# Performance work log

Measured on AMD Instinct MI355X. Metric: run time of the kernel, lower is better.

The kernel has to match this reference:

```python
import jax, jax.numpy as jnp
import numpy as np

D_MODEL = 1024
N_HEADS = 16
HEAD_DIM = D_MODEL // N_HEADS


def setup_inputs() -> dict:
    key = jax.random.key(0)
    ks = jax.random.split(key, 9)
    s = 1.0 / np.sqrt(D_MODEL)
    return {
        "x": jax.random.normal(ks[0], (4, 2048, D_MODEL), dtype=jnp.float32),
        "Wq": jax.random.normal(ks[1], (D_MODEL, D_MODEL), dtype=jnp.float32) * s,
        "bq": jax.random.normal(ks[2], (D_MODEL,), dtype=jnp.float32) * 0.01,
        "Wk": jax.random.normal(ks[3], (D_MODEL, D_MODEL), dtype=jnp.float32) * s,
        "bk": jax.random.normal(ks[4], (D_MODEL,), dtype=jnp.float32) * 0.01,
        "Wv": jax.random.normal(ks[5], (D_MODEL, D_MODEL), dtype=jnp.float32) * s,
        "bv": jax.random.normal(ks[6], (D_MODEL,), dtype=jnp.float32) * 0.01,
        "Wo": jax.random.normal(ks[7], (D_MODEL, D_MODEL), dtype=jnp.float32) * s,
        "bo": jax.random.normal(ks[8], (D_MODEL,), dtype=jnp.float32) * 0.01,
    }


def reference(x, Wq, bq, Wk, bk, Wv, bv, Wo, bo):
    b, s, d = x.shape  # [batch, seq, d_model]
    # projections (weights stored as [d_in, d_out], equiv to torch Linear W.T)
    q = x @ Wq + bq
    k = x @ Wk + bk
    v = x @ Wv + bv
    # split heads -> [b, h, s, hd]
    q = q.reshape(b, s, N_HEADS, HEAD_DIM).transpose(0, 2, 1, 3)
    k = k.reshape(b, s, N_HEADS, HEAD_DIM).transpose(0, 2, 1, 3)
    v = v.reshape(b, s, N_HEADS, HEAD_DIM).transpose(0, 2, 1, 3)
    scale = 1.0 / jnp.sqrt(jnp.asarray(HEAD_DIM, dtype=q.dtype))
    scores = jnp.einsum("bhqd,bhkd->bhqk", q, k) * scale  # [b,h,s,s]
    attn = jax.nn.softmax(scores, axis=-1)
    y = jnp.einsum("bhqk,bhkd->bhqd", attn, v)
    y = y.transpose(0, 2, 1, 3).reshape(b, s, d)
    return y @ Wo + bo
```

## Files before the change

### kernel.cpp

```cpp
#include <hip/hip_runtime.h>

#define SEQ   2048
#define DM    1024
#define NH    16
#define HD    64
#define MTOT  8192
#define QSCALE 0.18033688011112042f
#define SMAX  12.0f

typedef _Float16 f16x8 __attribute__((ext_vector_type(8)));
typedef float    f32x4 __attribute__((ext_vector_type(4)));

__device__ __forceinline__ unsigned short f2h(float f) {
    _Float16 h = (_Float16)f;
    return __builtin_bit_cast(unsigned short, h);
}
__device__ __forceinline__ float h2f(unsigned short u) {
    return (float)__builtin_bit_cast(_Float16, u);
}
__device__ __forceinline__ unsigned int pkrtz(float a, float b) {
    return __builtin_bit_cast(unsigned int, __builtin_amdgcn_cvt_pkrtz(a, b));
}
__device__ __forceinline__ float fexp2(float x) {
    return __builtin_amdgcn_exp2f(x);
}
__device__ __forceinline__ void async_cp16(const void* g, void* l) {
    __builtin_amdgcn_global_load_lds(
        (const __attribute__((address_space(1))) unsigned int*)g,
        (__attribute__((address_space(3))) unsigned int*)l, 16, 0, 0);
}

__global__ __launch_bounds__(256) void convert_x_kernel(
    const float* __restrict__ x, unsigned short* __restrict__ Xh)
{
    const size_t i8 = ((size_t)blockIdx.x * 256 + threadIdx.x) * 8;
    float f[8];
    *(float4*)&f[0] = *(const float4*)(x + i8);
    *(float4*)&f[4] = *(const float4*)(x + i8 + 4);
    unsigned short h[8];
#pragma unroll
    for (int e = 0; e < 8; ++e) h[e] = f2h(f[e]);
    uint4 ph;
    ph.x = h[0] | ((unsigned)h[1] << 16); ph.y = h[2] | ((unsigned)h[3] << 16);
    ph.z = h[4] | ((unsigned)h[5] << 16); ph.w = h[6] | ((unsigned)h[7] << 16);
    *(uint4*)(Xh + i8) = ph;
}

__global__ __launch_bounds__(256) void convert_w_kernel(
    const float* __restrict__ Wq, const float* __restrict__ Wk,
    const float* __restrict__ Wv, const float* __restrict__ Wo,
    unsigned short* __restrict__ WTh, unsigned short* __restrict__ WTl)
{
    __shared__ float tile[32][33];
    const int z = blockIdx.z;
    const float* W = (z == 0) ? Wq : (z == 1) ? Wk : (z == 2) ? Wv : Wo;
    const float s = (z == 0) ? QSCALE : 1.0f;
    const int r0 = blockIdx.y << 5, c0 = blockIdx.x << 5;
    const int tx = threadIdx.x, ty = threadIdx.y;
#pragma unroll
    for (int u = 0; u < 4; ++u)
        tile[ty + 8 * u][tx] = W[(size_t)(r0 + ty + 8 * u) * DM + c0 + tx];
    __syncthreads();
#pragma unroll
    for (int u = 0; u < 4; ++u) {
        const int dout = c0 + ty + 8 * u;
        const int din  = r0 + tx;
        const float v = tile[tx][ty + 8 * u] * s;
        const unsigned short hh = f2h(v);
        const size_t idx = (size_t)(z * DM + dout) * DM + din;
        WTh[idx] = hh;
        if (z == 3) WTl[idx] = f2h(v - h2f(hh));
    }
}

__global__ __launch_bounds__(256, 3) void gemm_kernel(
    const unsigned short* __restrict__ Agh, const unsigned short* __restrict__ Agl,
    const unsigned short* __restrict__ Bgh, const unsigned short* __restrict__ Bgl,
    const float* __restrict__ b0, const float* __restrict__ b1,
    const float* __restrict__ b2,
    float* __restrict__ Cf,
    unsigned short* __restrict__ Qf, unsigned short* __restrict__ Kf,
    unsigned short* __restrict__ Vt,
    const int mode)
{
    __shared__ unsigned short gsm[16384];

    const int t = threadIdx.x;
    const int wave = t >> 6, L = t & 63;
    const int quad = L >> 4, l16 = L & 15;
    const int m0 = blockIdx.x << 7, n0 = blockIdx.y << 7;

    const int trl = L >> 2;
    const int ck  = (L & 3) ^ (trl & 3);
    const unsigned short* gsrc;
    unsigned short* lb;
    int ub;
    if (mode == 1) {
        gsrc = (wave < 2) ? Agh : Bgh;
        ub   = (wave & 1) << 2;
        lb   = &gsm[((wave >> 1) << 13) + ((wave & 1) << 11)];
    } else {
        gsrc = (wave == 0) ? Agh : (wave == 1) ? Agl
             : (wave == 2) ? Bgh : Bgl;
        ub   = 0;
        lb   = &gsm[wave << 12];
    }
    const int rbase = (wave < 2) ? m0 : n0;
    const unsigned short* gl = gsrc + (size_t)(rbase + trl) * DM + ck * 8;

    const int wm = (wave >> 1) << 6, wn = (wave & 1) << 6;
    const int xk2 = l16 & 3;
    f32x4 acc[4][4] = {};

    for (int k0 = 0; k0 < DM; k0 += 32) {
        __syncthreads();
        if (mode == 1) {
#pragma unroll
            for (int u = 0; u < 4; ++u)
                async_cp16(gl + (size_t)(ub + u) * 16 * DM + k0, lb + (u << 9));
        } else {
#pragma unroll
            for (int u = 0; u < 8; ++u)
                async_cp16(gl + (size_t)u * 16 * DM + k0, lb + (u << 9));
        }
        __syncthreads();

        f16x8 fah[4], fal[4], fbh[4], fbl[4];
#pragma unroll
        for (int i = 0; i < 4; ++i) {
            const int ao = (wm + (i << 4) + l16) * 32 + ((quad ^ xk2) << 3);
            fah[i] = *(const f16x8*)&gsm[ao];
        }
#pragma unroll
        for (int j = 0; j < 4; ++j) {
            const int bo_ = (wn + (j << 4) + l16) * 32 + ((quad ^ xk2) << 3);
            fbh[j] = *(const f16x8*)&gsm[8192 + bo_];
        }
        if (mode == 0) {
#pragma unroll
            for (int i = 0; i < 4; ++i) {
                const int ao = (wm + (i << 4) + l16) * 32 + ((quad ^ xk2) << 3);
                fal[i] = *(const f16x8*)&gsm[4096 + ao];
            }
#pragma unroll
            for (int j = 0; j < 4; ++j) {
                const int bo_ = (wn + (j << 4) + l16) * 32 + ((quad ^ xk2) << 3);
                fbl[j] = *(const f16x8*)&gsm[12288 + bo_];
            }
        }
#pragma unroll
        for (int i = 0; i < 4; ++i)
#pragma unroll
            for (int j = 0; j < 4; ++j) {
                acc[i][j] = __builtin_amdgcn_mfma_f32_16x16x32_f16(fah[i], fbh[j], acc[i][j], 0, 0, 0);
                if (mode == 0) {
                    acc[i][j] = __builtin_amdgcn_mfma_f32_16x16x32_f16(fal[i], fbh[j], acc[i][j], 0, 0, 0);
                    acc[i][j] = __builtin_amdgcn_mfma_f32_16x16x32_f16(fah[i], fbl[j], acc[i][j], 0, 0, 0);
                }
            }
    }

    if (mode == 0) {
#pragma unroll
        for (int j = 0; j < 4; ++j) {
            const int col = n0 + wn + (j << 4) + l16;
            const float bj = b0[col];
#pragma unroll
            for (int i = 0; i < 4; ++i)
#pragma unroll
                for (int r = 0; r < 4; ++r) {
                    const int row = m0 + wm + (i << 4) + (quad << 2) + r;
                    Cf[(size_t)row * DM + col] = acc[i][j][r] + bj;
                }
        }
    } else {
#pragma unroll
        for (int j = 0; j < 4; ++j) {
            const int col = n0 + wn + (j << 4) + l16;
            const int seg = col >> 10;
            const int c = col & 1023;
            const int h_ = c >> 6, d_ = c & 63;
            const float bj = (seg == 0) ? b0[c] * QSCALE : (seg == 1) ? b1[c] : b2[c];
            unsigned short* Op = (seg == 0) ? Qf : Kf;
#pragma unroll
            for (int i = 0; i < 4; ++i) {
                const int row0 = m0 + wm + (i << 4) + (quad << 2);
                const int b_ = row0 >> 11, s0 = row0 & 2047;
                if (seg < 2) {
                    const size_t ib = ((size_t)b_ * NH + h_) * SEQ;
#pragma unroll
                    for (int r = 0; r < 4; ++r)
                        Op[(ib + s0 + r) * HD + d_] = f2h(acc[i][j][r] + bj);
                } else {
                    unsigned short e[4];
#pragma unroll
                    for (int r = 0; r < 4; ++r) e[r] = f2h(acc[i][j][r] + bj);
                    const size_t idx = (((size_t)b_ * NH + h_) * HD + d_) * SEQ + s0;
                    uint2 pv;
                    pv.x = e[0] | ((unsigned)e[1] << 16);
                    pv.y = e[2] | ((unsigned)e[3] << 16);
                    *(uint2*)&Vt[idx] = pv;
                }
            }
        }
    }
}

__global__ __launch_bounds__(256, 4) void attn_kernel(
    const unsigned short* __restrict__ Qg,
    const unsigned short* __restrict__ Kg,
    const unsigned short* __restrict__ Vg,
    unsigned short* __restrict__ Yh, unsigned short* __restrict__ Yl)
{
    __shared__ unsigned short smem[20480];

    const int t = threadIdx.x;
    const int wave = t >> 6, L = t & 63;
    const int quad = L >> 4, l16 = L & 15;
    const int xk = l16 & 7;
    const int bh = blockIdx.x;
    const int q0 = blockIdx.y << 7;
    const size_t base = (size_t)bh * SEQ * HD;

    f16x8 fQ[2][2];
#pragma unroll
    for (int nt = 0; nt < 2; ++nt) {
        const size_t qr = (size_t)(q0 + (wave << 5) + (nt << 4) + l16);
#pragma unroll
        for (int ks = 0; ks < 2; ++ks)
            fQ[nt][ks] = *(const f16x8*)(Qg + base + qr * HD + (ks << 5) + (quad << 3));
    }

    const int trl = L >> 3;
    const int sck = (L & 7) ^ trl;
    const unsigned short* sg = (wave == 0) ? Kg : Vg;
    const size_t rstr = (wave == 1) ? (size_t)SEQ : (size_t)HD;
    const unsigned short* gbase = sg + base + trl * rstr + sck * 8;

    float lsum[2] = {0.0f, 0.0f};
    f32x4 o[2][4] = {};
    f32x4 sacc[2][4];

    auto STAGE = [&](int kt) {
        if (wave < 2) {
            const size_t koff = (wave == 0) ? ((size_t)kt << 12) : ((size_t)kt << 6);
            unsigned short* lb = (wave == 0) ? smem
                                             : &smem[4096 + ((kt & 1) << 12)];
            const unsigned short* g = gbase + koff;
#pragma unroll
            for (int u = 0; u < 8; ++u)
                async_cp16(g + ((size_t)u << 3) * rstr, lb + (u << 9));
        }
    };
    auto QK = [&]() {
#pragma unroll
        for (int nt = 0; nt < 2; ++nt)
#pragma unroll
            for (int mt = 0; mt < 4; ++mt)
                sacc[nt][mt] = (f32x4){-SMAX, -SMAX, -SMAX, -SMAX};
        __builtin_amdgcn_s_setprio(1);
#pragma unroll
        for (int mt = 0; mt < 4; ++mt) {
#pragma unroll
            for (int ks = 0; ks < 2; ++ks) {
                const int off = ((mt << 4) + l16) * 64 + ((((ks << 2) + quad) ^ xk) << 3);
                const f16x8 fK = *(const f16x8*)&smem[off];
#pragma unroll
                for (int nt = 0; nt < 2; ++nt)
                    sacc[nt][mt] = __builtin_amdgcn_mfma_f32_16x16x32_f16(fK, fQ[nt][ks], sacc[nt][mt], 0, 0, 0);
            }
        }
        __builtin_amdgcn_s_setprio(0);
    };
    auto SMPV = [&](int ktp) {
        const int vb = 4096 + ((ktp & 1) << 12);
#pragma unroll
        for (int nt = 0; nt < 2; ++nt) {
            const int prow = (wave << 5) + (nt << 4) + l16;
#pragma unroll
            for (int mt = 0; mt < 4; ++mt) {
                float p[4];
#pragma unroll
                for (int r = 0; r < 4; ++r) {
                    p[r] = fexp2(sacc[nt][mt][r]);
                    lsum[nt] += p[r];
                }
                uint2 pk;
                pk.x = pkrtz(p[0], p[1]);
                pk.y = pkrtz(p[2], p[3]);
                const int ch = ((mt << 1) + (quad >> 1)) ^ xk;
                *(uint2*)&smem[12288 + prow * 64 + (ch << 3) + ((quad & 1) << 2)] = pk;
            }
        }
        f16x8 fV[4][2];
#pragma unroll
        for (int dt = 0; dt < 4; ++dt)
#pragma unroll
            for (int ks = 0; ks < 2; ++ks) {
                const int off = vb + ((dt << 4) + l16) * 64 + ((((ks << 2) + quad) ^ xk) << 3);
                fV[dt][ks] = *(const f16x8*)&smem[off];
            }
#pragma unroll
        for (int nt = 0; nt < 2; ++nt) {
            const int prow = (wave << 5) + (nt << 4) + l16;
            f16x8 fP[2];
#pragma unroll
            for (int ks = 0; ks < 2; ++ks) {
                const int off = 12288 + prow * 64 + ((((ks << 2) + quad) ^ xk) << 3);
                fP[ks] = *(const f16x8*)&smem[off];
            }
            __builtin_amdgcn_s_setprio(1);
#pragma unroll
            for (int dt = 0; dt < 4; ++dt)
#pragma unroll
                for (int ks = 0; ks < 2; ++ks)
                    o[nt][dt] = __builtin_amdgcn_mfma_f32_16x16x32_f16(fP[ks], fV[dt][ks], o[nt][dt], 0, 0, 0);
            __builtin_amdgcn_s_setprio(0);
        }
    };

    STAGE(0);
    __syncthreads();
    QK();

    for (int kt = 1; kt < 32; ++kt) {
        __syncthreads();
        STAGE(kt);
        SMPV(kt - 1);
        __syncthreads();
        QK();
    }
    SMPV(31);

#pragma unroll
    for (int nt = 0; nt < 2; ++nt) {
        lsum[nt] += __shfl_xor(lsum[nt], 16);
        lsum[nt] += __shfl_xor(lsum[nt], 32);
    }
    const int b_ = bh >> 4, h_ = bh & 15;
#pragma unroll
    for (int nt = 0; nt < 2; ++nt) {
        const float linv = 1.0f / lsum[nt];
        float lr[4];
#pragma unroll
        for (int r = 0; r < 4; ++r) lr[r] = __shfl(linv, (quad << 2) + r);
#pragma unroll
        for (int dt = 0; dt < 4; ++dt)
#pragma unroll
            for (int r = 0; r < 4; ++r) {
                const int row = q0 + (wave << 5) + (nt << 4) + (quad << 2) + r;
                const float v = o[nt][dt][r] * lr[r];
                const size_t idx = ((size_t)b_ * SEQ + row) * DM + (h_ << 6) + (dt << 4) + l16;
                const unsigned short hh = f2h(v);
                Yh[idx] = hh;
                Yl[idx] = f2h(v - h2f(hh));
            }
    }
}

extern "C" void kernel_launch(void* const* d_in, const int* in_sizes, int n_in,
                              void* d_out, int out_size, void* d_ws, size_t ws_size,
                              hipStream_t stream)
{
    const float* x  = (const float*)d_in[0];
    const float* Wq = (const float*)d_in[1];
    const float* bq = (const float*)d_in[2];
    const float* Wk = (const float*)d_in[3];
    const float* bk = (const float*)d_in[4];
    const float* Wv = (const float*)d_in[5];
    const float* bv = (const float*)d_in[6];
    const float* Wo = (const float*)d_in[7];
    const float* bo = (const float*)d_in[8];
    float* out = (float*)d_out;

    char* w = (char*)d_ws;
    unsigned short* Xh  = (unsigned short*)(w);
    unsigned short* Yl  = (unsigned short*)(w + (16u << 20));
    unsigned short* Qf  = (unsigned short*)(w + (32u << 20));
    unsigned short* Kf  = (unsigned short*)(w + (48u << 20));
    unsigned short* Vt  = (unsigned short*)(w + (64u << 20));
    unsigned short* WTh = (unsigned short*)(w + (112u << 20));
    unsigned short* WTl = (unsigned short*)(w + (120u << 20));
    unsigned short* Yh = Xh;

    convert_x_kernel<<<dim3(MTOT * DM / (256 * 8)), dim3(256), 0, stream>>>(x, Xh);
    convert_w_kernel<<<dim3(32, 32, 4), dim3(32, 8), 0, stream>>>(Wq, Wk, Wv, Wo, WTh, WTl);

    gemm_kernel<<<dim3(64, 24), dim3(256), 0, stream>>>(
        Xh, nullptr, WTh, nullptr, bq, bk, bv,
        nullptr, Qf, Kf, Vt, 1);

    attn_kernel<<<dim3(4 * NH, SEQ / 128), dim3(256), 0, stream>>>(
        Qf, Kf, Vt, Yh, Yl);

    gemm_kernel<<<dim3(64, 8), dim3(256), 0, stream>>>(
        Yh, Yl, WTh + (size_t)3072 * DM, WTl + (size_t)3072 * DM,
        bo, nullptr, nullptr,
        out, nullptr, nullptr, nullptr, 0);
}
```

Before: 299.3 us.

## Add dedicated double-buffered 256x128 QKV projection kernel with 512 threads

Replaces the mode-1 path of the shared GEMM kernel with a new QKV projection kernel. It uses 256x128 tiles, a K-step of 64 and 8 waves, and double-buffers shared memory (96KB dynamic) so the async copies for the next K tile overlap the MFMA work. It splits the A tile into two halves with barriers and raises wave priority around the MFMA bursts. The old GEMM kernel is specialised to the output projection only. The large shared-memory footprint limits occupancy, and the extra barriers may add synchronisation cost.

After: 298.7 us. Within noise of the previous version (-0.2%).

```diff
diff --git a/kernel.cpp b/kernel.cpp
--- a/kernel.cpp
+++ b/kernel.cpp
@@ -73,15 +73,154 @@
     }
 }
 
+__global__ __launch_bounds__(512, 2) void qkv_kernel(
+    const unsigned short* __restrict__ Ag,
+    const unsigned short* __restrict__ Bg,
+    const float* __restrict__ b0, const float* __restrict__ b1,
+    const float* __restrict__ b2,
+    unsigned short* __restrict__ Qf, unsigned short* __restrict__ Kf,
+    unsigned short* __restrict__ Vt)
+{
+    extern __shared__ unsigned short gsm[];
+
+    const int t = threadIdx.x;
+    const int wave = t >> 6, L = t & 63;
+    const int quad = L >> 4, l16 = L & 15;
+    const int xk = l16 & 7;
+    const int wr = wave >> 2, wc = wave & 3;
+    const int m0 = blockIdx.x << 8;
+    const int n0 = blockIdx.y << 7;
+
+    const int srow = L >> 3;
+    const int sck  = (L & 7) ^ srow;
+
+    f32x4 acc[8][2] = {};
+
+    #define STAGE_A(buf, half, k0)                                              \
+        _Pragma("unroll")                                                       \
+        for (int u = 0; u < 2; ++u)                                             \
+            async_cp16(Ag + (size_t)(m0 + (half)*128 + wave*16 + u*8 + srow) * DM \
+                          + (k0) + sck*8,                                       \
+                       &gsm[(buf)*16384 + (half)*8192 + wave*1024 + u*512]);
+    #define STAGE_B(buf, k0)                                                    \
+        _Pragma("unroll")                                                       \
+        for (int u = 0; u < 2; ++u)                                             \
+            async_cp16(Bg + (size_t)(n0 + wave*16 + u*8 + srow) * DM            \
+                          + (k0) + sck*8,                                       \
+                       &gsm[32768 + (buf)*8192 + wave*1024 + u*512]);
+
+    STAGE_A(0, 0, 0);
+    STAGE_A(0, 1, 0);
+    STAGE_B(0, 0);
+    __syncthreads();
+
+    for (int tk = 0; tk < 16; ++tk) {
+        const int cur = tk & 1, nxt = cur ^ 1;
+        const int k1 = (tk + 1) << 6;
+        const int abase = cur * 16384 + wr * 8192;
+        const int bbase = 32768 + cur * 8192;
+
+        if (tk < 15) {
+            STAGE_A(nxt, 0, k1);
+            STAGE_B(nxt, k1);
+        }
+        f16x8 fb[2][2];
+#pragma unroll
+        for (int j = 0; j < 2; ++j)
+#pragma unroll
+            for (int ks = 0; ks < 2; ++ks)
+                fb[j][ks] = *(const f16x8*)&gsm[bbase
+                    + ((wc << 5) + (j << 4) + l16) * 64
+                    + ((((ks << 2) + quad) ^ xk) << 3)];
+        {
+            f16x8 fa[4][2];
+#pragma unroll
+            for (int i = 0; i < 4; ++i)
+#pragma unroll
+                for (int ks = 0; ks < 2; ++ks)
+                    fa[i][ks] = *(const f16x8*)&gsm[abase
+                        + ((i << 4) + l16) * 64
+                        + ((((ks << 2) + quad) ^ xk) << 3)];
+            __builtin_amdgcn_s_barrier();
+            __builtin_amdgcn_s_setprio(1);
+#pragma unroll
+            for (int i = 0; i < 4; ++i)
+#pragma unroll
+                for (int j = 0; j < 2; ++j)
+#pragma unroll
+                    for (int ks = 0; ks < 2; ++ks)
+                        acc[i][j] = __builtin_amdgcn_mfma_f32_16x16x32_f16(
+                            fa[i][ks], fb[j][ks], acc[i][j], 0, 0, 0);
+            __builtin_amdgcn_s_setprio(0);
+            __builtin_amdgcn_s_barrier();
+        }
+
+        if (tk < 15) {
+            STAGE_A(nxt, 1, k1);
+        }
+        {
+            f16x8 fa[4][2];
+#pragma unroll
+            for (int i = 0; i < 4; ++i)
+#pragma unroll
+                for (int ks = 0; ks < 2; ++ks)
+                    fa[i][ks] = *(const f16x8*)&gsm[abase
+                        + ((64 + (i << 4) + l16)) * 64
+                        + ((((ks << 2) + quad) ^ xk) << 3)];
+            __builtin_amdgcn_s_barrier();
+            __builtin_amdgcn_s_setprio(1);
+#pragma unroll
+            for (int i = 0; i < 4; ++i)
+#pragma unroll
+                for (int j = 0; j < 2; ++j)
+#pragma unroll
+                    for (int ks = 0; ks < 2; ++ks)
+                        acc[4 + i][j] = __builtin_amdgcn_mfma_f32_16x16x32_f16(
+                            fa[i][ks], fb[j][ks], acc[4 + i][j], 0, 0, 0);
+            __builtin_amdgcn_s_setprio(0);
+        }
+
+        __syncthreads();
+    }
+    #undef STAGE_A
+    #undef STAGE_B
+
+#pragma unroll
+    for (int j = 0; j < 2; ++j) {
+        const int col = n0 + (wc << 5) + (j << 4) + l16;
+        const int seg = col >> 10;
+        const int c = col & 1023;
+        const int h_ = c >> 6, d_ = c & 63;
+        const float bj = (seg == 0) ? b0[c] * QSCALE : (seg == 1) ? b1[c] : b2[c];
+        unsigned short* Op = (seg == 0) ? Qf : Kf;
+#pragma unroll
+        for (int i8 = 0; i8 < 8; ++i8) {
+            const int row0 = m0 + (wr << 7) + (i8 << 4) + (quad << 2);
+            const int b_ = row0 >> 11, s0 = row0 & 2047;
+            if (seg < 2) {
+                const size_t ib = ((size_t)b_ * NH + h_) * SEQ;
+#pragma unroll
+                for (int r = 0; r < 4; ++r)
+                    Op[(ib + s0 + r) * HD + d_] = f2h(acc[i8][j][r] + bj);
+            } else {
+                unsigned short e[4];
+#pragma unroll
+                for (int r = 0; r < 4; ++r) e[r] = f2h(acc[i8][j][r] + bj);
+                const size_t idx = (((size_t)b_ * NH + h_) * HD + d_) * SEQ + s0;
+                uint2 pv;
+                pv.x = e[0] | ((unsigned)e[1] << 16);
+                pv.y = e[2] | ((unsigned)e[3] << 16);
+                *(uint2*)&Vt[idx] = pv;
+            }
+        }
+    }
+}
+
 __global__ __launch_bounds__(256, 3) void gemm_kernel(
     const unsigned short* __restrict__ Agh, const unsigned short* __restrict__ Agl,
     const unsigned short* __restrict__ Bgh, const unsigned short* __restrict__ Bgl,
-    const float* __restrict__ b0, const float* __restrict__ b1,
-    const float* __restrict__ b2,
-    float* __restrict__ Cf,
-    unsigned short* __restrict__ Qf, unsigned short* __restrict__ Kf,
-    unsigned short* __restrict__ Vt,
-    const int mode)
+    const float* __restrict__ b0,
+    float* __restrict__ Cf)
 {
     __shared__ unsigned short gsm[16384];
 
@@ -92,21 +231,11 @@
 
     const int trl = L >> 2;
     const int ck  = (L & 3) ^ (trl & 3);
-    const unsigned short* gsrc;
-    unsigned short* lb;
-    int ub;
-    if (mode == 1) {
-        gsrc = (wave < 2) ? Agh : Bgh;
-        ub   = (wave & 1) << 2;
-        lb   = &gsm[((wave >> 1) << 13) + ((wave & 1) << 11)];
-    } else {
-        gsrc = (wave == 0) ? Agh : (wave == 1) ? Agl
-             : (wave == 2) ? Bgh : Bgl;
-        ub   = 0;
-        lb   = &gsm[wave << 12];
-    }
+    const unsigned short* gsrc = (wave == 0) ? Agh : (wave == 1) ? Agl
+                               : (wave == 2) ? Bgh : Bgl;
     const int rbase = (wave < 2) ? m0 : n0;
     const unsigned short* gl = gsrc + (size_t)(rbase + trl) * DM + ck * 8;
+    unsigned short* lb = &gsm[wave << 12];
 
     const int wm = (wave >> 1) << 6, wn = (wave & 1) << 6;
     const int xk2 = l16 & 3;
@@ -114,15 +243,9 @@
 
     for (int k0 = 0; k0 < DM; k0 += 32) {
         __syncthreads();
-        if (mode == 1) {
-#pragma unroll
-            for (int u = 0; u < 4; ++u)
-                async_cp16(gl + (size_t)(ub + u) * 16 * DM + k0, lb + (u << 9));
-        } else {
-#pragma unroll
-            for (int u = 0; u < 8; ++u)
-                async_cp16(gl + (size_t)u * 16 * DM + k0, lb + (u << 9));
-        }
+#pragma unroll
+        for (int u = 0; u < 8; ++u)
+            async_cp16(gl + (size_t)u * 16 * DM + k0, lb + (u << 9));
         __syncthreads();
 
         f16x8 fah[4], fal[4], fbh[4], fbl[4];
@@ -130,79 +253,35 @@
         for (int i = 0; i < 4; ++i) {
             const int ao = (wm + (i << 4) + l16) * 32 + ((quad ^ xk2) << 3);
             fah[i] = *(const f16x8*)&gsm[ao];
+            fal[i] = *(const f16x8*)&gsm[4096 + ao];
         }
 #pragma unroll
         for (int j = 0; j < 4; ++j) {
             const int bo_ = (wn + (j << 4) + l16) * 32 + ((quad ^ xk2) << 3);
             fbh[j] = *(const f16x8*)&gsm[8192 + bo_];
-        }
-        if (mode == 0) {
-#pragma unroll
-            for (int i = 0; i < 4; ++i) {
-                const int ao = (wm + (i << 4) + l16) * 32 + ((quad ^ xk2) << 3);
-                fal[i] = *(const f16x8*)&gsm[4096 + ao];
-            }
-#pragma unroll
-            for (int j = 0; j < 4; ++j) {
-                const int bo_ = (wn + (j << 4) + l16) * 32 + ((quad ^ xk2) << 3);
-                fbl[j] = *(const f16x8*)&gsm[12288 + bo_];
-            }
+            fbl[j] = *(const f16x8*)&gsm[12288 + bo_];
         }
 #pragma unroll
         for (int i = 0; i < 4; ++i)
 #pragma unroll
             for (int j = 0; j < 4; ++j) {
                 acc[i][j] = __builtin_amdgcn_mfma_f32_16x16x32_f16(fah[i], fbh[j], acc[i][j], 0, 0, 0);
-                if (mode == 0) {
-                    acc[i][j] = __builtin_amdgcn_mfma_f32_16x16x32_f16(fal[i], fbh[j], acc[i][j], 0, 0, 0);
-                    acc[i][j] = __builtin_amdgcn_mfma_f32_16x16x32_f16(fah[i], fbl[j], acc[i][j], 0, 0, 0);
-                }
-            }
-    }
-
-    if (mode == 0) {
-#pragma unroll
-        for (int j = 0; j < 4; ++j) {
-            const int col = n0 + wn + (j << 4) + l16;
-            const float bj = b0[col];
-#pragma unroll
-            for (int i = 0; i < 4; ++i)
-#pragma unroll
-                for (int r = 0; r < 4; ++r) {
-                    const int row = m0 + wm + (i << 4) + (quad << 2) + r;
-                    Cf[(size_t)row * DM + col] = acc[i][j][r] + bj;
-                }
-        }
-    } else {
-#pragma unroll
-        for (int j = 0; j < 4; ++j) {
-            const int col = n0 + wn + (j << 4) + l16;
-            const int seg = col >> 10;
-            const int c = col & 1023;
-            const int h_ = c >> 6, d_ = c & 63;
-            const float bj = (seg == 0) ? b0[c] * QSCALE : (seg == 1) ? b1[c] : b2[c];
-            unsigned short* Op = (seg == 0) ? Qf : Kf;
-#pragma unroll
-            for (int i = 0; i < 4; ++i) {
-                const int row0 = m0 + wm + (i << 4) + (quad << 2);
-                const int b_ = row0 >> 11, s0 = row0 & 2047;
-                if (seg < 2) {
-                    const size_t ib = ((size_t)b_ * NH + h_) * SEQ;
-#pragma unroll
-                    for (int r = 0; r < 4; ++r)
-                        Op[(ib + s0 + r) * HD + d_] = f2h(acc[i][j][r] + bj);
-                } else {
-                    unsigned short e[4];
-#pragma unroll
-                    for (int r = 0; r < 4; ++r) e[r] = f2h(acc[i][j][r] + bj);
-                    const size_t idx = (((size_t)b_ * NH + h_) * HD + d_) * SEQ + s0;
-                    uint2 pv;
-                    pv.x = e[0] | ((unsigned)e[1] << 16);
-                    pv.y = e[2] | ((unsigned)e[3] << 16);
-                    *(uint2*)&Vt[idx] = pv;
-                }
-            }
-        }
+                acc[i][j] = __builtin_amdgcn_mfma_f32_16x16x32_f16(fal[i], fbh[j], acc[i][j], 0, 0, 0);
+                acc[i][j] = __builtin_amdgcn_mfma_f32_16x16x32_f16(fah[i], fbl[j], acc[i][j], 0, 0, 0);
+            }
+    }
+
+#pragma unroll
+    for (int j = 0; j < 4; ++j) {
+        const int col = n0 + wn + (j << 4) + l16;
+        const float bj = b0[col];
+#pragma unroll
+        for (int i = 0; i < 4; ++i)
+#pragma unroll
+            for (int r = 0; r < 4; ++r) {
+                const int row = m0 + wm + (i << 4) + (quad << 2) + r;
+                Cf[(size_t)row * DM + col] = acc[i][j][r] + bj;
+            }
     }
 }
 
@@ -383,18 +462,19 @@
     unsigned short* WTl = (unsigned short*)(w + (120u << 20));
     unsigned short* Yh = Xh;
 
+    hipFuncSetAttribute(reinterpret_cast<const void*>(qkv_kernel),
+                        hipFuncAttributeMaxDynamicSharedMemorySize, 98304);
+
     convert_x_kernel<<<dim3(MTOT * DM / (256 * 8)), dim3(256), 0, stream>>>(x, Xh);
     convert_w_kernel<<<dim3(32, 32, 4), dim3(32, 8), 0, stream>>>(Wq, Wk, Wv, Wo, WTh, WTl);
 
-    gemm_kernel<<<dim3(64, 24), dim3(256), 0, stream>>>(
-        Xh, nullptr, WTh, nullptr, bq, bk, bv,
-        nullptr, Qf, Kf, Vt, 1);
+    qkv_kernel<<<dim3(32, 24), dim3(512), 98304, stream>>>(
+        Xh, WTh, bq, bk, bv, Qf, Kf, Vt);
 
     attn_kernel<<<dim3(4 * NH, SEQ / 128), dim3(256), 0, stream>>>(
         Qf, Kf, Vt, Yh, Yl);
 
     gemm_kernel<<<dim3(64, 8), dim3(256), 0, stream>>>(
         Yh, Yl, WTh + (size_t)3072 * DM, WTl + (size_t)3072 * DM,
-        bo, nullptr, nullptr,
-        out, nullptr, nullptr, nullptr, 0);
-}
+        bo, out);
+}
```
